# Kernel tuning notes

Measured on AMD Instinct MI355X. Metric: run time of the kernel, lower is better.

The kernel has to match this reference:

```python
import jax, jax.numpy as jnp
import numpy as np

EMBED_DIM = 1024
NUM_HEADS = 16
HEAD_DIM = EMBED_DIM // NUM_HEADS
MLP_HIDDEN = 4096
B, S = 2, 2048


def setup_inputs() -> dict:
    key = jax.random.key(0)
    ks = jax.random.split(key, 10)
    sd = lambda fan_in: 1.0 / np.sqrt(fan_in)
    x = jax.random.normal(ks[0], (B, S, EMBED_DIM), dtype=jnp.float32)
    # weights stored (in, out) so y = x @ W + b (same math as torch Linear)
    w_qkv = jax.random.normal(ks[1], (EMBED_DIM, 3 * EMBED_DIM), jnp.float32) * sd(EMBED_DIM)
    w_proj = jax.random.normal(ks[2], (EMBED_DIM, EMBED_DIM), jnp.float32) * sd(EMBED_DIM)
    b_proj = jnp.zeros((EMBED_DIM,), jnp.float32)
    w_fc1 = jax.random.normal(ks[3], (EMBED_DIM, MLP_HIDDEN), jnp.float32) * sd(EMBED_DIM)
    b_fc1 = jnp.zeros((MLP_HIDDEN,), jnp.float32)
    w_fc2 = jax.random.normal(ks[4], (MLP_HIDDEN, EMBED_DIM), jnp.float32) * sd(MLP_HIDDEN)
    b_fc2 = jnp.zeros((EMBED_DIM,), jnp.float32)
    g1 = jnp.ones((EMBED_DIM,), jnp.float32)
    be1 = jnp.zeros((EMBED_DIM,), jnp.float32)
    g2 = jnp.ones((EMBED_DIM,), jnp.float32)
    be2 = jnp.zeros((EMBED_DIM,), jnp.float32)
    return {"x": x, "w_qkv": w_qkv, "w_proj": w_proj, "b_proj": b_proj,
            "w_fc1": w_fc1, "b_fc1": b_fc1, "w_fc2": w_fc2, "b_fc2": b_fc2,
            "g1": g1, "be1": be1, "g2": g2, "be2": be2}


def _layernorm(x, g, b, eps=1e-5):
    mu = jnp.mean(x, axis=-1, keepdims=True)
    var = jnp.var(x, axis=-1, keepdims=True)
    return (x - mu) * jax.lax.rsqrt(var + eps) * g + b


def _block(x, w_qkv, w_proj, b_proj, w_fc1, b_fc1, w_fc2, b_fc2, g1, be1, g2, be2):
    # --- attention branch ---
    h = _layernorm(x, g1, be1)
    qkv = h @ w_qkv  # [B,S,3D]
    qkv = qkv.reshape(B, S, 3, NUM_HEADS, HEAD_DIM).transpose(2, 0, 3, 1, 4)
    q, k, v = qkv[0], qkv[1], qkv[2]  # each [B,H,S,Dh]
    scale = 1.0 / np.sqrt(HEAD_DIM).astype(np.float32)
    dots = jnp.einsum('bhqd,bhkd->bhqk', q, k) * scale  # naive full score matrix
    attn = jax.nn.softmax(dots, axis=-1)
    out = jnp.einsum('bhqk,bhkd->bhqd', attn, v)
    out = out.transpose(0, 2, 1, 3).reshape(B, S, EMBED_DIM)
    x = x + (out @ w_proj + b_proj)
    # --- mlp branch ---
    h2 = _layernorm(x, g2, be2)
    mlp = jax.nn.gelu(h2 @ w_fc1 + b_fc1, approximate=False) @ w_fc2 + b_fc2
    return x + mlp


def reference(x, w_qkv, w_proj, b_proj, w_fc1, b_fc1, w_fc2, b_fc2, g1, be1, g2, be2):
    return _block(x, w_qkv, w_proj, b_proj, w_fc1, b_fc1, w_fc2, b_fc2, g1, be1, g2, be2)
```

## Files before the change

### kernel.cpp

```cpp
#include <hip/hip_runtime.h>

typedef __attribute__((ext_vector_type(8))) short short8;
typedef __attribute__((ext_vector_type(4))) float f32x4;

#define MFMA16(a, b, c) __builtin_amdgcn_mfma_f32_16x16x32_bf16((a), (b), (c), 0, 0, 0)

static __device__ __forceinline__ unsigned short f2bf(float f) {
    unsigned int u = __float_as_uint(f);
    return (unsigned short)((u + 0x7fffu + ((u >> 16) & 1u)) >> 16);
}

static __device__ __forceinline__ void glds16(const unsigned short* g, unsigned short* l) {
    __builtin_amdgcn_global_load_lds(
        (const __attribute__((address_space(1))) unsigned int*)g,
        (__attribute__((address_space(3))) unsigned int*)l, 16, 0, 0);
}

__global__ __launch_bounds__(256) void convt_all_kernel(
    const float* __restrict__ w_qkv, const float* __restrict__ w_proj,
    const float* __restrict__ w_fc1, const float* __restrict__ w_fc2,
    unsigned short* __restrict__ wqkvT, unsigned short* __restrict__ wprojT,
    unsigned short* __restrict__ wfc1T, unsigned short* __restrict__ wfc2T) {
    __shared__ unsigned short Ts[32][33];
    int id = blockIdx.x;
    const float* W; unsigned short* WT; int K, N, bx, by;
    if (id < 3072)      { W = w_qkv;  WT = wqkvT;  K = 1024; N = 3072; bx = id % 96;  by = id / 96; }
    else if (id < 4096) { id -= 3072; W = w_proj; WT = wprojT; K = 1024; N = 1024; bx = id & 31; by = id >> 5; }
    else if (id < 8192) { id -= 4096; W = w_fc1;  WT = wfc1T;  K = 1024; N = 4096; bx = id & 127; by = id >> 7; }
    else                { id -= 8192; W = w_fc2;  WT = wfc2T;  K = 4096; N = 1024; bx = id & 31; by = id >> 5; }
    int t = threadIdx.x;
    int bk = by * 32, bn = bx * 32;
    int r = t >> 3, c = (t & 7) * 4;
    float4 w = *(const float4*)&W[(size_t)(bk + r) * N + bn + c];
    Ts[c + 0][r] = f2bf(w.x); Ts[c + 1][r] = f2bf(w.y);
    Ts[c + 2][r] = f2bf(w.z); Ts[c + 3][r] = f2bf(w.w);
    __syncthreads();
    ushort4 o;
    o.x = Ts[r][c]; o.y = Ts[r][c + 1]; o.z = Ts[r][c + 2]; o.w = Ts[r][c + 3];
    *(ushort4*)&WT[(size_t)(bn + r) * K + bk + c] = o;
}

__global__ __launch_bounds__(256) void ln_kernel(const float* __restrict__ x,
                                                 const float* __restrict__ g,
                                                 const float* __restrict__ be,
                                                 unsigned short* __restrict__ y) {
    int row = blockIdx.x;
    const float* xr = x + (size_t)row * 1024;
    unsigned short* yr = y + (size_t)row * 1024;
    int t = threadIdx.x;
    float v[4];
    float sum = 0.f, sq = 0.f;
#pragma unroll
    for (int i = 0; i < 4; ++i) {
        float f = xr[t + i * 256];
        v[i] = f; sum += f; sq += f * f;
    }
#pragma unroll
    for (int o = 32; o > 0; o >>= 1) { sum += __shfl_down(sum, o); sq += __shfl_down(sq, o); }
    __shared__ float red[8];
    int wave = t >> 6, lane = t & 63;
    if (lane == 0) { red[wave] = sum; red[4 + wave] = sq; }
    __syncthreads();
    sum = red[0] + red[1] + red[2] + red[3];
    sq  = red[4] + red[5] + red[6] + red[7];
    float mean = sum * (1.f / 1024.f);
    float var  = sq * (1.f / 1024.f) - mean * mean;
    float rstd = rsqrtf(var + 1e-5f);
#pragma unroll
    for (int i = 0; i < 4; ++i) {
        int c = t + i * 256;
        yr[c] = f2bf((v[i] - mean) * rstd * g[c] + be[c]);
    }
}

template <int BN>
__global__ __launch_bounds__(256) void gemm_kernel(const unsigned short* __restrict__ A,
                                                   const unsigned short* __restrict__ BT,
                                                   const float* __restrict__ bias,
                                                   const float* __restrict__ resid,
                                                   void* __restrict__ C,
                                                   int M, int N, int K, int act, int cF32) {
    constexpr int NT = BN / 32;
    __shared__ __align__(16) unsigned short As[2][128][32];
    __shared__ __align__(16) unsigned short Bs[2][BN][32];
    int t = threadIdx.x, wave = t >> 6, lane = t & 63;
    int lm = lane & 15, quad = lane >> 4, k8 = quad * 8;
    int wm = (wave >> 1) * 64, wn = (wave & 1) * (BN / 2);

    int id = blockIdx.y * gridDim.x + blockIdx.x;
    int gsz = gridDim.x * 8;
    int grp = id / gsz, rem = id % gsz;
    int br = (grp * 8 + (rem & 7)) * 128;
    int bc = (rem >> 3) * BN;

    int srow = lane >> 2, scol = (lane & 3) * 8;
    const unsigned short* Ag0 = A + (size_t)(br + wave * 32 + srow) * K + scol;
    const unsigned short* Ag1 = Ag0 + (size_t)16 * K;
    const unsigned short* Bg0 = BT + (size_t)(bc + wave * (BN / 4) + srow) * K + scol;
    const unsigned short* Bg1 = Bg0 + (size_t)16 * K;

    f32x4 zero4 = {0.f, 0.f, 0.f, 0.f};
    f32x4 acc[4][NT];
#pragma unroll
    for (int i = 0; i < 4; ++i)
#pragma unroll
        for (int j = 0; j < NT; ++j) acc[i][j] = zero4;

    for (int k0 = 0; k0 < K; k0 += 64) {
        __syncthreads();
#pragma unroll
        for (int s = 0; s < 2; ++s) {
            int ko = k0 + s * 32;
            glds16(Ag0 + ko, &As[s][wave * 32][0]);
            glds16(Ag1 + ko, &As[s][wave * 32 + 16][0]);
            glds16(Bg0 + ko, &Bs[s][wave * (BN / 4)][0]);
            if (BN == 128) glds16(Bg1 + ko, &Bs[s][wave * (BN / 4) + 16][0]);
        }
        __syncthreads();
#pragma unroll
        for (int s = 0; s < 2; ++s) {
            short8 af[4], bf[NT];
#pragma unroll
            for (int i = 0; i < 4; ++i) af[i] = *(const short8*)&As[s][wm + i * 16 + lm][k8];
#pragma unroll
            for (int j = 0; j < NT; ++j) bf[j] = *(const short8*)&Bs[s][wn + j * 16 + lm][k8];
#pragma unroll
            for (int i = 0; i < 4; ++i)
#pragma unroll
                for (int j = 0; j < NT; ++j) acc[i][j] = MFMA16(af[i], bf[j], acc[i][j]);
        }
    }

#pragma unroll
    for (int i = 0; i < 4; ++i)
#pragma unroll
        for (int j = 0; j < NT; ++j) {
            int col = bc + wn + j * 16 + lm;
            float bv = bias ? bias[col] : 0.f;
#pragma unroll
            for (int r = 0; r < 4; ++r) {
                int row = br + wm + i * 16 + quad * 4 + r;
                float v = acc[i][j][r] + bv;
                if (act == 1) v = 0.5f * v * (1.f + erff(v * 0.70710678118f));
                size_t idx = (size_t)row * N + col;
                if (resid) v += resid[idx];
                if (cF32) ((float*)C)[idx] = v;
                else ((unsigned short*)C)[idx] = f2bf(v);
            }
        }
}

__global__ __launch_bounds__(256) void kvprep_kernel(const unsigned short* __restrict__ qkv,
                                                     unsigned short* __restrict__ Kp,
                                                     unsigned short* __restrict__ Vt) {
    __shared__ unsigned short Vl[64][72];
    int t = threadIdx.x;
    int w = blockIdx.x, bh = blockIdx.y;
    int b = bh >> 4, h = bh & 15;
    int kt = w * 64;
    int sl = t >> 2, c = (t & 3) * 16;
    const unsigned short* src = qkv + (size_t)(b * 2048 + kt + sl) * 3072 + h * 64 + c;
    {
        uint4 k0 = *(const uint4*)(src + 1024);
        uint4 k1 = *(const uint4*)(src + 1024 + 8);
        int sw = sl & 7;
        int o0 = (c >> 3), o1 = o0 + 1;
        unsigned short* krow = Kp + ((size_t)bh * 2048 + kt + sl) * 64;
        *(uint4*)&krow[(o0 ^ sw) << 3] = k0;
        *(uint4*)&krow[(o1 ^ sw) << 3] = k1;
    }
    {
        uint4 v0 = *(const uint4*)(src + 2048);
        uint4 v1 = *(const uint4*)(src + 2048 + 8);
        *(uint4*)&Vl[sl][c] = v0;
        *(uint4*)&Vl[sl][c + 8] = v1;
    }
    __syncthreads();
    {
        int d = t >> 2, kc = (t & 3) * 16;
        unsigned short vv[16];
#pragma unroll
        for (int i = 0; i < 16; ++i) vv[i] = Vl[kc + i][d];
        int sw = d & 7;
        int ko0 = kc >> 3, ko1 = ko0 + 1;
        unsigned short* vrow = Vt + ((((size_t)bh * 32 + w) * 64) + d) * 64;
        *(uint4*)&vrow[(ko0 ^ sw) << 3] = *(uint4*)&vv[0];
        *(uint4*)&vrow[(ko1 ^ sw) << 3] = *(uint4*)&vv[8];
    }
}

__global__ __launch_bounds__(256) void attn2_kernel(const unsigned short* __restrict__ qkv,
                                                    const unsigned short* __restrict__ Kp,
                                                    const unsigned short* __restrict__ Vt,
                                                    unsigned short* __restrict__ out) {
    __shared__ __align__(16) unsigned short Qs[64][72];
    __shared__ __align__(16) unsigned short Ks[4096];
    __shared__ __align__(16) unsigned short Vs[4096];
    __shared__ __align__(16) unsigned short Ps[4][16][72];

    int t = threadIdx.x, wave = t >> 6, lane = t & 63;
    int lm = lane & 15, quad = lane >> 4, k8 = quad * 8;
    int bh = blockIdx.y, b = bh >> 4, h = bh & 15;
    int q0 = blockIdx.x * 64;
    const unsigned short* base = qkv + (size_t)b * 2048 * 3072 + h * 64;

    {
        int r = t >> 2, c = (t & 3) * 16;
        const unsigned short* src = base + (size_t)(q0 + r) * 3072 + c;
        *(uint4*)&Qs[r][c] = *(const uint4*)src;
        *(uint4*)&Qs[r][c + 8] = *(const uint4*)(src + 8);
    }
    __syncthreads();
    short8 qa0 = *(const short8*)&Qs[wave * 16 + lm][k8];
    short8 qa1 = *(const short8*)&Qs[wave * 16 + lm][32 + k8];

    f32x4 zero4 = {0.f, 0.f, 0.f, 0.f};
    f32x4 oacc[4] = {zero4, zero4, zero4, zero4};
    float lsum[4] = {0.f, 0.f, 0.f, 0.f};

    for (int kt = 0; kt < 2048; kt += 64) {
        __syncthreads();
        {
            const unsigned short* kg = Kp + ((size_t)bh * 2048 + kt) * 64 + wave * 1024 + (lane << 3);
            unsigned short* kl = &Ks[wave * 1024];
            glds16(kg, kl);
            glds16(kg + 512, kl + 512);
            const unsigned short* vg = Vt + (((size_t)bh * 32 + (kt >> 6)) * 64) * 64 + wave * 1024 + (lane << 3);
            unsigned short* vl = &Vs[wave * 1024];
            glds16(vg, vl);
            glds16(vg + 512, vl + 512);
        }
        __syncthreads();

        f32x4 s[4];
#pragma unroll
        for (int nt = 0; nt < 4; ++nt) {
            int key = nt * 16 + lm;
            int swk = lm & 7;
            const unsigned short* krow = &Ks[key * 64];
            short8 kf0 = *(const short8*)&krow[(quad ^ swk) << 3];
            short8 kf1 = *(const short8*)&krow[((quad ^ swk) ^ 4) << 3];
            f32x4 a = zero4;
            a = MFMA16(qa0, kf0, a);
            a = MFMA16(qa1, kf1, a);
            s[nt] = a;
        }

#pragma unroll
        for (int r = 0; r < 4; ++r) {
            int row = quad * 4 + r;
            int sw = (row >> 1) & 7;
#pragma unroll
            for (int nt = 0; nt < 4; ++nt) {
                float p = __expf(s[nt][r] * 0.125f - 8.0f);
                lsum[r] += p;
                int g = (nt << 1) + (lm >> 3);
                Ps[wave][row][((g ^ sw) << 3) + (lm & 7)] = f2bf(p);
            }
        }

#pragma unroll
        for (int kh = 0; kh < 2; ++kh) {
            int pg = (kh << 2) + quad;
            short8 pa = *(const short8*)&Ps[wave][lm][(pg ^ ((lm >> 1) & 7)) << 3];
#pragma unroll
            for (int nt = 0; nt < 4; ++nt) {
                int d = nt * 16 + lm;
                short8 vf = *(const short8*)&Vs[d * 64 + ((pg ^ (lm & 7)) << 3)];
                oacc[nt] = MFMA16(pa, vf, oacc[nt]);
            }
        }
    }

#pragma unroll
    for (int r = 0; r < 4; ++r) {
        float l = lsum[r];
        l += __shfl_xor(l, 1); l += __shfl_xor(l, 2);
        l += __shfl_xor(l, 4); l += __shfl_xor(l, 8);
        float inv = 1.f / l;
        int qrow = q0 + wave * 16 + quad * 4 + r;
        size_t o = ((size_t)(b * 2048 + qrow)) * 1024 + h * 64;
#pragma unroll
        for (int nt = 0; nt < 4; ++nt) out[o + nt * 16 + lm] = f2bf(oacc[nt][r] * inv);
    }
}

__global__ __launch_bounds__(256) void attn_kernel(const unsigned short* __restrict__ qkv,
                                                   unsigned short* __restrict__ out) {
    __shared__ __align__(16) unsigned short Qs[64][72];
    __shared__ __align__(16) unsigned short Ks[64][72];
    __shared__ __align__(16) unsigned short Vs[64][72];
    __shared__ __align__(16) unsigned short Ps[4][16][72];
    int t = threadIdx.x, wave = t >> 6, lane = t & 63;
    int lm = lane & 15, quad = lane >> 4, k8 = quad * 8;
    int bh = blockIdx.y, b = bh >> 4, h = bh & 15;
    int q0 = blockIdx.x * 64;
    const unsigned short* base = qkv + (size_t)b * 2048 * 3072 + h * 64;
    const unsigned short* kb = base + 1024;
    const unsigned short* vb = base + 2048;
    {
        int r = t >> 2, c = (t & 3) * 16;
        const unsigned short* src = base + (size_t)(q0 + r) * 3072 + c;
        *(uint4*)&Qs[r][c] = *(const uint4*)src;
        *(uint4*)&Qs[r][c + 8] = *(const uint4*)(src + 8);
    }
    __syncthreads();
    short8 qa0 = *(const short8*)&Qs[wave * 16 + lm][k8];
    short8 qa1 = *(const short8*)&Qs[wave * 16 + lm][32 + k8];
    f32x4 zero4 = {0.f, 0.f, 0.f, 0.f};
    f32x4 oacc[4] = {zero4, zero4, zero4, zero4};
    float lsum[4] = {0.f, 0.f, 0.f, 0.f};
    int sr = t >> 2, sc = (t & 3) * 16;
    for (int kt = 0; kt < 2048; kt += 64) {
        __syncthreads();
        {
            const unsigned short* ksrc = kb + (size_t)(kt + sr) * 3072 + sc;
            *(uint4*)&Ks[sr][sc] = *(const uint4*)ksrc;
            *(uint4*)&Ks[sr][sc + 8] = *(const uint4*)(ksrc + 8);
            const unsigned short* vsrc = vb + (size_t)(kt + sr) * 3072 + sc;
            unsigned short tv[16] __attribute__((aligned(16)));
            *(uint4*)&tv[0] = *(const uint4*)vsrc;
            *(uint4*)&tv[8] = *(const uint4*)(vsrc + 8);
            int kg = sr >> 3, kw = sr & 7;
#pragma unroll
            for (int j = 0; j < 16; ++j) {
                int d = sc + j;
                Vs[d][((kg ^ ((d >> 3) & 7)) << 3) + kw] = tv[j];
            }
        }
        __syncthreads();
        f32x4 s[4];
#pragma unroll
        for (int nt = 0; nt < 4; ++nt) {
            short8 kf0 = *(const short8*)&Ks[nt * 16 + lm][k8];
            short8 kf1 = *(const short8*)&Ks[nt * 16 + lm][32 + k8];
            f32x4 a = zero4;
            a = MFMA16(qa0, kf0, a);
            a = MFMA16(qa1, kf1, a);
            s[nt] = a;
        }
#pragma unroll
        for (int r = 0; r < 4; ++r) {
            int row = quad * 4 + r;
            int sw = (row >> 1) & 7;
#pragma unroll
            for (int nt = 0; nt < 4; ++nt) {
                float p = __expf(s[nt][r] * 0.125f - 8.0f);
                lsum[r] += p;
                int g = (nt << 1) + (lm >> 3);
                Ps[wave][row][((g ^ sw) << 3) + (lm & 7)] = f2bf(p);
            }
        }
#pragma unroll
        for (int kh = 0; kh < 2; ++kh) {
            int pg = (kh << 2) + quad;
            short8 pa = *(const short8*)&Ps[wave][lm][(pg ^ ((lm >> 1) & 7)) << 3];
#pragma unroll
            for (int nt = 0; nt < 4; ++nt) {
                int d = nt * 16 + lm;
                short8 vf = *(const short8*)&Vs[d][(pg ^ ((d >> 3) & 7)) << 3];
                oacc[nt] = MFMA16(pa, vf, oacc[nt]);
            }
        }
    }
#pragma unroll
    for (int r = 0; r < 4; ++r) {
        float l = lsum[r];
        l += __shfl_xor(l, 1); l += __shfl_xor(l, 2);
        l += __shfl_xor(l, 4); l += __shfl_xor(l, 8);
        float inv = 1.f / l;
        int qrow = q0 + wave * 16 + quad * 4 + r;
        size_t o = ((size_t)(b * 2048 + qrow)) * 1024 + h * 64;
#pragma unroll
        for (int nt = 0; nt < 4; ++nt) out[o + nt * 16 + lm] = f2bf(oacc[nt][r] * inv);
    }
}

extern "C" void kernel_launch(void* const* d_in, const int* in_sizes, int n_in,
                              void* d_out, int out_size, void* d_ws, size_t ws_size,
                              hipStream_t stream) {
    const float* x      = (const float*)d_in[0];
    const float* w_qkv  = (const float*)d_in[1];
    const float* w_proj = (const float*)d_in[2];
    const float* b_proj = (const float*)d_in[3];
    const float* w_fc1  = (const float*)d_in[4];
    const float* b_fc1  = (const float*)d_in[5];
    const float* w_fc2  = (const float*)d_in[6];
    const float* b_fc2  = (const float*)d_in[7];
    const float* g1     = (const float*)d_in[8];
    const float* be1    = (const float*)d_in[9];
    const float* g2     = (const float*)d_in[10];
    const float* be2    = (const float*)d_in[11];
    float* out = (float*)d_out;
    unsigned short* sb = (unsigned short*)d_out;

    char* ws = (char*)d_ws;
    unsigned short* wqkvT  = (unsigned short*)ws;
    unsigned short* wprojT = (unsigned short*)(ws + ((size_t)6u << 20));
    unsigned short* wfc1T  = (unsigned short*)(ws + ((size_t)8u << 20));
    unsigned short* wfc2T  = (unsigned short*)(ws + ((size_t)16u << 20));
    unsigned short* qkv    = (unsigned short*)(ws + ((size_t)24u << 20));

    convt_all_kernel<<<dim3(12288), dim3(256), 0, stream>>>(
        w_qkv, w_proj, w_fc1, w_fc2, wqkvT, wprojT, wfc1T, wfc2T);
    ln_kernel<<<dim3(4096), dim3(256), 0, stream>>>(x, g1, be1, sb);
    gemm_kernel<128><<<dim3(24, 32), dim3(256), 0, stream>>>(
        sb, wqkvT, nullptr, nullptr, qkv, 4096, 3072, 1024, 0, 0);

    if (ws_size >= ((size_t)72u << 20)) {
        unsigned short* Kp = (unsigned short*)(ws + ((size_t)48u << 20));
        unsigned short* Vt = (unsigned short*)(ws + ((size_t)56u << 20));
        float*          x2 = (float*)(ws + ((size_t)24u << 20));
        unsigned short* m1 = (unsigned short*)(ws + ((size_t)40u << 20));
        kvprep_kernel<<<dim3(32, 32), dim3(256), 0, stream>>>(qkv, Kp, Vt);
        attn2_kernel<<<dim3(32, 32), dim3(256), 0, stream>>>(qkv, Kp, Vt, sb);
        gemm_kernel<64><<<dim3(16, 32), dim3(256), 0, stream>>>(
            sb, wprojT, b_proj, x, x2, 4096, 1024, 1024, 0, 1);
        ln_kernel<<<dim3(4096), dim3(256), 0, stream>>>(x2, g2, be2, sb);
        gemm_kernel<128><<<dim3(32, 32), dim3(256), 0, stream>>>(
            sb, wfc1T, b_fc1, nullptr, m1, 4096, 4096, 1024, 1, 0);
        gemm_kernel<64><<<dim3(16, 32), dim3(256), 0, stream>>>(
            m1, wfc2T, b_fc2, x2, out, 4096, 1024, 4096, 0, 1);
    } else {
        float*          x2  = (float*)(ws + ((size_t)24u << 20));
        unsigned short* m1c = (unsigned short*)(ws + ((size_t)40u << 20));
        unsigned short* h2  = (unsigned short*)d_out + ((size_t)4u << 20);
        attn_kernel<<<dim3(32, 32), dim3(256), 0, stream>>>(qkv, sb);
        gemm_kernel<64><<<dim3(16, 32), dim3(256), 0, stream>>>(
            sb, wprojT, b_proj, x, x2, 4096, 1024, 1024, 0, 1);
        ln_kernel<<<dim3(4096), dim3(256), 0, stream>>>(x2, g2, be2, h2);
        for (int c = 0; c < 4; ++c) {
            size_t ro = (size_t)c * 1024;
            gemm_kernel<128><<<dim3(32, 8), dim3(256), 0, stream>>>(
                h2 + ro * 1024, wfc1T, b_fc1, nullptr, m1c, 1024, 4096, 1024, 1, 0);
            gemm_kernel<64><<<dim3(16, 8), dim3(256), 0, stream>>>(
                m1c, wfc2T, b_fc2, x2 + ro * 1024, out + ro * 1024, 1024, 1024, 4096, 0, 1);
        }
    }
}
```

Baseline: 424.0 us.

## Double-buffer GEMM K-loop with async LDS prefetch and XOR-swizzled LDS layout

```diff
diff --git a/kernel.cpp b/kernel.cpp
--- a/kernel.cpp
+++ b/kernel.cpp
@@ -84,7 +84,7 @@
     __shared__ __align__(16) unsigned short As[2][128][32];
     __shared__ __align__(16) unsigned short Bs[2][BN][32];
     int t = threadIdx.x, wave = t >> 6, lane = t & 63;
-    int lm = lane & 15, quad = lane >> 4, k8 = quad * 8;
+    int lm = lane & 15, quad = lane >> 4;
     int wm = (wave >> 1) * 64, wn = (wave & 1) * (BN / 2);
 
     int id = blockIdx.y * gridDim.x + blockIdx.x;
@@ -93,7 +93,8 @@
     int br = (grp * 8 + (rem & 7)) * 128;
     int bc = (rem >> 3) * BN;
 
-    int srow = lane >> 2, scol = (lane & 3) * 8;
+    int srow = lane >> 2;
+    int scol = ((lane & 3) ^ ((srow >> 1) & 3)) * 8;
     const unsigned short* Ag0 = A + (size_t)(br + wave * 32 + srow) * K + scol;
     const unsigned short* Ag1 = Ag0 + (size_t)16 * K;
     const unsigned short* Bg0 = BT + (size_t)(bc + wave * (BN / 4) + srow) * K + scol;
@@ -106,29 +107,39 @@
 #pragma unroll
         for (int j = 0; j < NT; ++j) acc[i][j] = zero4;
 
-    for (int k0 = 0; k0 < K; k0 += 64) {
-        __syncthreads();
-#pragma unroll
-        for (int s = 0; s < 2; ++s) {
-            int ko = k0 + s * 32;
-            glds16(Ag0 + ko, &As[s][wave * 32][0]);
-            glds16(Ag1 + ko, &As[s][wave * 32 + 16][0]);
-            glds16(Bg0 + ko, &Bs[s][wave * (BN / 4)][0]);
-            if (BN == 128) glds16(Bg1 + ko, &Bs[s][wave * (BN / 4) + 16][0]);
-        }
-        __syncthreads();
-#pragma unroll
-        for (int s = 0; s < 2; ++s) {
-            short8 af[4], bf[NT];
-#pragma unroll
-            for (int i = 0; i < 4; ++i) af[i] = *(const short8*)&As[s][wm + i * 16 + lm][k8];
-#pragma unroll
-            for (int j = 0; j < NT; ++j) bf[j] = *(const short8*)&Bs[s][wn + j * 16 + lm][k8];
-#pragma unroll
-            for (int i = 0; i < 4; ++i)
-#pragma unroll
-                for (int j = 0; j < NT; ++j) acc[i][j] = MFMA16(af[i], bf[j], acc[i][j]);
-        }
+    auto stage = [&](int buf, int ko) {
+        glds16(Ag0 + ko, &As[buf][wave * 32][0]);
+        glds16(Ag1 + ko, &As[buf][wave * 32 + 16][0]);
+        glds16(Bg0 + ko, &Bs[buf][wave * (BN / 4)][0]);
+        if (BN == 128) glds16(Bg1 + ko, &Bs[buf][wave * (BN / 4) + 16][0]);
+    };
+
+    int nt = K >> 5;
+    stage(0, 0);
+    int rsw = (lm >> 1) & 3;
+    int cq = (quad ^ rsw) << 3;
+    for (int tt = 0; tt < nt; ++tt) {
+        int cur = tt & 1;
+        if (tt + 1 < nt) {
+            stage(cur ^ 1, (tt + 1) << 5);
+            if (BN == 128) asm volatile("s_waitcnt vmcnt(4)" ::: "memory");
+            else           asm volatile("s_waitcnt vmcnt(3)" ::: "memory");
+        } else {
+            asm volatile("s_waitcnt vmcnt(0)" ::: "memory");
+        }
+        __builtin_amdgcn_s_barrier();
+        __builtin_amdgcn_sched_barrier(0);
+        short8 af[4], bf[NT];
+#pragma unroll
+        for (int i = 0; i < 4; ++i) af[i] = *(const short8*)&As[cur][wm + i * 16 + lm][cq];
+#pragma unroll
+        for (int j = 0; j < NT; ++j) bf[j] = *(const short8*)&Bs[cur][wn + j * 16 + lm][cq];
+#pragma unroll
+        for (int i = 0; i < 4; ++i)
+#pragma unroll
+            for (int j = 0; j < NT; ++j) acc[i][j] = MFMA16(af[i], bf[j], acc[i][j]);
+        __builtin_amdgcn_sched_barrier(0);
+        __builtin_amdgcn_s_barrier();
     }
 
 #pragma unroll
```

After: 416.9 us. Within noise of the previous version (-1.7%).
